# Optimization experiments

Measured on AMD Instinct MI355X. Metric: run time of the kernel, lower is better.

The kernel has to match this reference:

```python
import jax, jax.numpy as jnp
import numpy as np

N = 50000
E = 1600000
IN_DIM = 256
HID = 64
OUT = 16
NEG_SLOPE = 0.01


def setup_inputs() -> dict:
    key = jax.random.key(0)
    ks = jax.random.split(key, 6)
    local_features = jax.random.normal(ks[0], (N, IN_DIM), dtype=jnp.float32)
    edge_index = jax.random.randint(ks[1], (2, E), 0, N, dtype=jnp.int32)
    W0 = jax.random.normal(ks[2], (IN_DIM, HID), dtype=jnp.float32) * 0.05
    a0 = jax.random.normal(ks[3], (2 * HID, 1), dtype=jnp.float32) * 0.05
    W1 = jax.random.normal(ks[4], (HID, OUT), dtype=jnp.float32) * 0.05
    a1 = jax.random.normal(ks[5], (2 * OUT, 1), dtype=jnp.float32) * 0.05
    return {"local_features": local_features, "edge_index": edge_index,
            "W0": W0, "a0": a0, "W1": W1, "a1": a1}


def _segment_softmax(scores, seg, num_segments):
    # softmax over edges sharing the same row (destination) id
    smax = jax.ops.segment_max(scores, seg, num_segments=num_segments)
    ex = jnp.exp(scores - smax[seg])
    ssum = jax.ops.segment_sum(ex, seg, num_segments=num_segments)
    return ex / ssum[seg]


def _gat_layer(H, row, col, W, a, apply_elu):
    d = W.shape[1]
    Hw = H @ W                                   # [N, d]
    # score_e = leaky_relu([Hw[row] || Hw[col]] @ a) = leaky_relu(pr[row] + pc[col])
    pr = Hw @ a[:d, 0]                           # [N]
    pc = Hw @ a[d:, 0]                           # [N]
    s = pr[row] + pc[col]                        # [E]
    s = jnp.where(s >= 0, s, NEG_SLOPE * s)      # leaky_relu
    att = _segment_softmax(s, row, Hw.shape[0])  # per-row sparse softmax (dim=1)
    # out[row] = sum_e att_e * Hw[col_e]
    out = jax.ops.segment_sum(att[:, None] * Hw[col], row, num_segments=Hw.shape[0])
    if apply_elu:
        out = jnp.where(out > 0, out, jnp.expm1(out))  # elu
    return out


def reference(local_features, edge_index, W0, a0, W1, a1):
    row = edge_index[0]
    col = edge_index[1]
    H = _gat_layer(local_features, row, col, W0, a0, apply_elu=True)
    H = _gat_layer(H, row, col, W1, a1, apply_elu=False)
    return jax.nn.log_softmax(H, axis=1)
```

## Files before the change

### kernel.cpp

```cpp
#include <hip/hip_runtime.h>
#include <hip/hip_bf16.h>
#include <math.h>

#define NN 50000
#define NE 1600000
#define BSH 9
#define BCK 98
#define BCAP 20480

typedef __attribute__((ext_vector_type(8))) short bf16x8;
typedef __attribute__((ext_vector_type(4))) float f32x4;
typedef __attribute__((ext_vector_type(2))) float f32x2;

__device__ __forceinline__ short f2bf(float f) {
    return (short)((__float_as_uint(f) + 0x8000u) >> 16);
}
__device__ __forceinline__ float lo16(unsigned u) { return __uint_as_float(u << 16); }
__device__ __forceinline__ float hi16(unsigned u) { return __uint_as_float(u & 0xffff0000u); }
__device__ __forceinline__ unsigned enc_f(float f) {
    unsigned u = __float_as_uint(f);
    return (u & 0x80000000u) ? ~u : (u | 0x80000000u);
}
__device__ __forceinline__ float dec_f(unsigned e) {
    return (e & 0x80000000u) ? __uint_as_float(e & 0x7FFFFFFFu)
                             : __uint_as_float(~e);
}

__global__ void setup_kernel(int* __restrict__ gcursor, unsigned* __restrict__ maxes,
                             const float* __restrict__ W, ushort* __restrict__ WTg) {
    int b = blockIdx.x;
    int t = threadIdx.x;
    if (b == 0) {
        if (t < BCK) gcursor[t] = t * BCAP;
        if (t < 2) maxes[t] = 0u;
    } else {
        int i = (b - 1) * 256 + t;
        int n = i >> 8, k = i & 255;
        WTg[n * 264 + k] = (ushort)f2bf(W[k * 64 + n]);
    }
}

__global__ void __launch_bounds__(1024) binA_kernel(
        const int* __restrict__ row, const int* __restrict__ col,
        int* __restrict__ gcursor, unsigned* __restrict__ staging) {
    __shared__ unsigned lds_stage[8192];
    __shared__ unsigned lds_addr[8192];
    __shared__ int lds_cnt[128];
    __shared__ int lds_off[128];
    __shared__ int wg_goff[128];
    __shared__ int wtot[2];
    int t = threadIdx.x;
    int lane = t & 63;
    int w = t >> 6;

    for (int cb = blockIdx.x * 8192; cb < NE; cb += gridDim.x * 8192) {
        int cnt_edges = NE - cb; if (cnt_edges > 8192) cnt_edges = 8192;
        if (t < 128) lds_cnt[t] = 0;
        __syncthreads();
        int myb[8]; int mylo[8]; unsigned mypk[8];
        int e0 = cb + t * 8;
        if (t * 8 + 7 < cnt_edges) {
            int4 r0 = *(const int4*)(row + e0);
            int4 r1 = *(const int4*)(row + e0 + 4);
            int4 c0 = *(const int4*)(col + e0);
            int4 c1 = *(const int4*)(col + e0 + 4);
            int rr[8] = {r0.x, r0.y, r0.z, r0.w, r1.x, r1.y, r1.z, r1.w};
            int cc[8] = {c0.x, c0.y, c0.z, c0.w, c1.x, c1.y, c1.z, c1.w};
            #pragma unroll
            for (int i = 0; i < 8; ++i) {
                int b = rr[i] >> BSH;
                myb[i] = b;
                mypk[i] = ((unsigned)(rr[i] & 511) << 16) | (unsigned)cc[i];
                mylo[i] = atomicAdd(&lds_cnt[b], 1);
            }
        } else {
            #pragma unroll
            for (int i = 0; i < 8; ++i) {
                int idx = t * 8 + i;
                myb[i] = -1;
                if (idx < cnt_edges) {
                    int e = cb + idx;
                    int r = row[e], c = col[e];
                    myb[i] = r >> BSH;
                    mypk[i] = ((unsigned)(r & 511) << 16) | (unsigned)c;
                    mylo[i] = atomicAdd(&lds_cnt[myb[i]], 1);
                }
            }
        }
        __syncthreads();
        int v = (t < 128) ? lds_cnt[t] : 0;
        int x = v;
        #pragma unroll
        for (int off = 1; off < 64; off <<= 1) {
            int y = __shfl_up(x, off);
            if (lane >= off) x += y;
        }
        if (t < 128 && lane == 63) wtot[w] = x;
        __syncthreads();
        int add = (w == 1) ? wtot[0] : 0;
        if (t < 128) lds_off[t] = x - v + add;
        if (t < BCK) {
            int cc2 = lds_cnt[t];
            wg_goff[t] = cc2 ? atomicAdd(&gcursor[t], cc2) : 0;
        }
        __syncthreads();
        #pragma unroll
        for (int i = 0; i < 8; ++i) if (myb[i] >= 0) {
            int p = lds_off[myb[i]] + mylo[i];
            lds_stage[p] = mypk[i];
            lds_addr[p] = (unsigned)(wg_goff[myb[i]] + mylo[i]);
        }
        __syncthreads();
        for (int i = t; i < cnt_edges; i += 1024)
            staging[lds_addr[i]] = lds_stage[i];
        __syncthreads();
    }
}

__global__ void __launch_bounds__(1024) binB_kernel(
        const int* __restrict__ gcursor,
        const unsigned* __restrict__ staging,
        int* __restrict__ rowptr,
        ushort* __restrict__ colperm) {
    __shared__ int bsc[128];
    __shared__ int bw[2];
    __shared__ int cur[512];
    __shared__ int wls8[8];
    __shared__ ushort lds_col[BCAP];
    int b = blockIdx.x;
    int t = threadIdx.x;
    int lane = t & 63;
    int w = t >> 6;

    if (t < 128) {
        int v = 0;
        if (t < BCK) {
            v = gcursor[t] - t * BCAP;
            if (v > BCAP) v = BCAP;
        }
        int x = v;
        #pragma unroll
        for (int off = 1; off < 64; off <<= 1) {
            int y = __shfl_up(x, off);
            if (lane >= off) x += y;
        }
        if (lane == 63) bw[w] = x;
        bsc[t] = x - v;
    }
    __syncthreads();
    int gbase = bsc[b] + ((b >= 64) ? bw[0] : 0);
    int cnt = gcursor[b] - b * BCAP;
    if (cnt > BCAP) cnt = BCAP;
    if (b == 0 && t == 0) rowptr[NN] = bw[0] + bw[1];
    int rbase = b << BSH;
    int nrows = NN - rbase; if (nrows > 512) nrows = 512;
    const unsigned* sb = staging + (size_t)b * BCAP;

    unsigned ev[20];
    #pragma unroll
    for (int j = 0; j < 5; ++j) {
        int i0 = t * 4 + j * 4096;
        uint4 val = {0u, 0u, 0u, 0u};
        if (i0 + 3 < cnt) {
            val = *(const uint4*)(sb + i0);
        } else {
            if (i0 + 0 < cnt) val.x = sb[i0 + 0];
            if (i0 + 1 < cnt) val.y = sb[i0 + 1];
            if (i0 + 2 < cnt) val.z = sb[i0 + 2];
            if (i0 + 3 < cnt) val.w = sb[i0 + 3];
        }
        ev[j * 4 + 0] = val.x; ev[j * 4 + 1] = val.y;
        ev[j * 4 + 2] = val.z; ev[j * 4 + 3] = val.w;
    }

    if (t < 512) cur[t] = 0;
    __syncthreads();
    #pragma unroll
    for (int j = 0; j < 5; ++j) {
        #pragma unroll
        for (int l = 0; l < 4; ++l) {
            int idx = t * 4 + j * 4096 + l;
            if (idx < cnt) atomicAdd(&cur[ev[j * 4 + l] >> 16], 1);
        }
    }
    __syncthreads();
    int v = 0, x = 0;
    if (t < 512) {
        v = cur[t];
        x = v;
        #pragma unroll
        for (int off = 1; off < 64; off <<= 1) {
            int y = __shfl_up(x, off);
            if (lane >= off) x += y;
        }
        if (lane == 63) wls8[w] = x;
    }
    __syncthreads();
    if (t < 8) {
        int s = wls8[t];
        #pragma unroll
        for (int off = 1; off < 8; off <<= 1) {
            int y = __shfl_up(s, off, 8);
            if ((t & 7) >= off) s += y;
        }
        wls8[t] = s;
    }
    __syncthreads();
    int excl = 0;
    if (t < 512) {
        excl = x - v + ((w > 0) ? wls8[w - 1] : 0);
        if (t < nrows) rowptr[rbase + t] = gbase + excl;
    }
    __syncthreads();
    if (t < 512) cur[t] = excl;
    __syncthreads();
    #pragma unroll
    for (int j = 0; j < 5; ++j) {
        #pragma unroll
        for (int l = 0; l < 4; ++l) {
            int idx = t * 4 + j * 4096 + l;
            if (idx < cnt) {
                unsigned e = ev[j * 4 + l];
                int pos = atomicAdd(&cur[e >> 16], 1);
                lds_col[pos] = (ushort)(e & 0xFFFFu);
            }
        }
    }
    __syncthreads();
    for (int i = t; i < cnt; i += 1024)
        colperm[gbase + i] = lds_col[i];
}

__global__ void pcmax_kernel(const float* __restrict__ pc, unsigned* __restrict__ out) {
    int i = blockIdx.x * 256 + threadIdx.x;
    float v = (i < NN) ? pc[i] : -1e30f;
    #pragma unroll
    for (int off = 32; off; off >>= 1) v = fmaxf(v, __shfl_xor(v, off));
    if ((threadIdx.x & 63) == 0) atomicMax(out, enc_f(v));
}

__global__ void __launch_bounds__(256) gemm0_kernel(
        const float* __restrict__ X,
        const ushort* __restrict__ WTg,
        const float* __restrict__ a,
        __hip_bfloat16* __restrict__ Hwb,
        float* __restrict__ pr,
        float* __restrict__ pc,
        unsigned* __restrict__ max0) {
    __shared__ ushort Wt[64 * 264];
    __shared__ unsigned bmax;
    int tid = threadIdx.x;
    if (tid == 0) bmax = 0u;
    {
        const uint* src = (const uint*)WTg;
        uint* dst = (uint*)Wt;
        for (int i = tid; i < 64 * 132; i += 256) dst[i] = src[i];
    }
    __syncthreads();
    int lane = tid & 63, wid = tid >> 6;
    int c = lane & 15, quad = lane >> 4;
    const ushort* wtp[4];
#pragma unroll
    for (int g = 0; g < 4; ++g) wtp[g] = &Wt[(g * 16 + c) * 264 + quad * 8];
    float aA[4], aB[4];
#pragma unroll
    for (int g = 0; g < 4; ++g) { aA[g] = a[g * 16 + c]; aB[g] = a[64 + g * 16 + c]; }

    int row0 = blockIdx.x * 128 + wid * 16;
    float qmax = -1e30f;

#pragma unroll
    for (int tt = 0; tt < 2; ++tt) {
        int rt = row0 + tt * 64;
        int arow = rt + c; if (arow >= NN) arow = NN - 1;
        const float* xbase = X + (size_t)arow * 256 + quad * 8;
        f32x4 acc[4];
#pragma unroll
        for (int g = 0; g < 4; ++g) acc[g] = (f32x4){0.f, 0.f, 0.f, 0.f};

#pragma unroll
        for (int k0 = 0; k0 < 256; k0 += 32) {
            float4 xa = *(const float4*)(xbase + k0);
            float4 xb = *(const float4*)(xbase + k0 + 4);
            bf16x8 af;
            af[0] = f2bf(xa.x); af[1] = f2bf(xa.y); af[2] = f2bf(xa.z); af[3] = f2bf(xa.w);
            af[4] = f2bf(xb.x); af[5] = f2bf(xb.y); af[6] = f2bf(xb.z); af[7] = f2bf(xb.w);
#pragma unroll
            for (int g = 0; g < 4; ++g) {
                bf16x8 bg = *(const bf16x8*)(wtp[g] + k0);
                acc[g] = __builtin_amdgcn_mfma_f32_16x16x32_bf16(af, bg, acc[g], 0, 0, 0);
            }
        }

#pragma unroll
        for (int r = 0; r < 4; ++r) {
            int row = rt + quad * 4 + r;
            float v0 = acc[0][r], v1 = acc[1][r], v2 = acc[2][r], v3 = acc[3][r];
            if (row < NN) {
                __hip_bfloat16* hp = Hwb + (size_t)row * 64 + c;
                hp[0]  = __float2bfloat16(v0);
                hp[16] = __float2bfloat16(v1);
                hp[32] = __float2bfloat16(v2);
                hp[48] = __float2bfloat16(v3);
            }
            float pv = v0 * aA[0] + v1 * aA[1] + v2 * aA[2] + v3 * aA[3];
            float qv = v0 * aB[0] + v1 * aB[1] + v2 * aB[2] + v3 * aB[3];
#pragma unroll
            for (int off = 8; off; off >>= 1) {
                pv += __shfl_xor(pv, off);
                qv += __shfl_xor(qv, off);
            }
            if (c == 0 && row < NN) { pr[row] = pv; pc[row] = qv; }
            if (row < NN) qmax = fmaxf(qmax, qv);
        }
    }
    qmax = fmaxf(qmax, __shfl_xor(qmax, 16));
    qmax = fmaxf(qmax, __shfl_xor(qmax, 32));
    if (lane == 0) atomicMax(&bmax, enc_f(qmax));
    __syncthreads();
    if (tid == 0) atomicMax(max0, bmax);
}

__global__ void __launch_bounds__(256) node0_kernel(
        const int* __restrict__ rowptr,
        const ushort* __restrict__ colperm,
        const float* __restrict__ pr,
        const float* __restrict__ pc,
        const unsigned* __restrict__ pcmax,
        const ushort* __restrict__ Hwb,
        const float* __restrict__ W1,
        const float* __restrict__ a1,
        __hip_bfloat16* __restrict__ Hw1b,
        float* __restrict__ pr1,
        float* __restrict__ pc1) {
    __shared__ float W1s[64 * 17];
    __shared__ float a1s[32];
    __shared__ float hbuf[4][64];
    __shared__ unsigned long long wcbuf[4][64];
    int t = threadIdx.x;
    for (int i = t; i < 64 * 16; i += 256)
        W1s[(i >> 4) * 17 + (i & 15)] = W1[i];
    if (t < 32) a1s[t] = a1[t];
    __syncthreads();

    int lane = t & 63;
    int wid = t >> 6;
    int node = blockIdx.x * 4 + wid;
    int k = lane & 15, q = lane >> 4;
    int start = rowptr[node], end = rowptr[node + 1];
    float pri = pr[node];
    float m = pri + dec_f(*pcmax);
    m = (m >= 0.f) ? m : 0.01f * m;

    float wsum = 0.f;
    f32x2 accA = {0.f, 0.f}, accB = {0.f, 0.f};
    for (int base = start; base < end; base += 64) {
        int n = end - base; if (n > 64) n = 64;
        float wv = 0.f; unsigned cv = 0;
        if (lane < n) {
            cv = (unsigned)colperm[base + lane];
            float s = pri + pc[cv];
            s = (s >= 0.f) ? s : 0.01f * s;
            wv = __expf(s - m);
        }
        wsum += wv;
        wcbuf[wid][lane] = ((unsigned long long)cv << 32) |
                           (unsigned long long)__float_as_uint(wv);
        int iters = (n + 3) >> 2;
        #pragma unroll 4
        for (int jj = 0; jj < iters; ++jj) {
            unsigned long long wc = wcbuf[wid][jj * 4 + q];
            float wj = __uint_as_float((unsigned)wc);
            int cj = (int)(wc >> 32);
            uint2 hv = *(const uint2*)(Hwb + (size_t)cj * 64 + k * 4);
            f32x2 wj2 = {wj, wj};
            f32x2 h01 = {lo16(hv.x), hi16(hv.x)};
            f32x2 h23 = {lo16(hv.y), hi16(hv.y)};
            accA += wj2 * h01;
            accB += wj2 * h23;
        }
    }
#pragma unroll
    for (int off = 32; off; off >>= 1) wsum += __shfl_xor(wsum, off);
    float acc0 = accA.x, acc1 = accA.y, acc2 = accB.x, acc3 = accB.y;
    acc0 += __shfl_xor(acc0, 16); acc0 += __shfl_xor(acc0, 32);
    acc1 += __shfl_xor(acc1, 16); acc1 += __shfl_xor(acc1, 32);
    acc2 += __shfl_xor(acc2, 16); acc2 += __shfl_xor(acc2, 32);
    acc3 += __shfl_xor(acc3, 16); acc3 += __shfl_xor(acc3, 32);

    float inv = (wsum > 0.f) ? 1.f / wsum : 0.f;
    float h0 = acc0 * inv; h0 = (h0 > 0.f) ? h0 : (__expf(h0) - 1.f);
    float h1 = acc1 * inv; h1 = (h1 > 0.f) ? h1 : (__expf(h1) - 1.f);
    float h2 = acc2 * inv; h2 = (h2 > 0.f) ? h2 : (__expf(h2) - 1.f);
    float h3 = acc3 * inv; h3 = (h3 > 0.f) ? h3 : (__expf(h3) - 1.f);
    if (q == 0) {
        float4 hh = {h0, h1, h2, h3};
        *(float4*)&hbuf[wid][k * 4] = hh;
    }
    int j = lane & 15, p = lane >> 4;
    const float* hbp = hbuf[wid];
    float vj = 0.f;
#pragma unroll
    for (int i = 0; i < 16; ++i) {
        int kk = p * 16 + i;
        vj = fmaf(hbp[kk], W1s[kk * 17 + j], vj);
    }
    vj += __shfl_xor(vj, 16);
    vj += __shfl_xor(vj, 32);
    if (p == 0) Hw1b[(size_t)node * 16 + j] = __float2bfloat16(vj);
    float pv = vj * a1s[j];
    float qv = vj * a1s[16 + j];
#pragma unroll
    for (int off = 8; off; off >>= 1) {
        pv += __shfl_xor(pv, off);
        qv += __shfl_xor(qv, off);
    }
    if (lane == 0) { pr1[node] = pv; pc1[node] = qv; }
}

__global__ void __launch_bounds__(256) node1_kernel(
        const int* __restrict__ rowptr,
        const ushort* __restrict__ colperm,
        const float* __restrict__ pr,
        const float* __restrict__ pc,
        const unsigned* __restrict__ pcmax,
        const ushort* __restrict__ Hwb,
        float* __restrict__ out) {
    __shared__ unsigned long long wcbuf[4][64];
    int lane = threadIdx.x & 63;
    int wid = threadIdx.x >> 6;
    int node = blockIdx.x * 4 + wid;
    int k = lane & 7, q = lane >> 3;
    int start = rowptr[node], end = rowptr[node + 1];
    float pri = pr[node];
    float m = pri + dec_f(*pcmax);
    m = (m >= 0.f) ? m : 0.01f * m;

    float wsum = 0.f;
    f32x2 acc = {0.f, 0.f};
    for (int base = start; base < end; base += 64) {
        int n = end - base; if (n > 64) n = 64;
        float wv = 0.f; unsigned cv = 0;
        if (lane < n) {
            cv = (unsigned)colperm[base + lane];
            float s = pri + pc[cv];
            s = (s >= 0.f) ? s : 0.01f * s;
            wv = __expf(s - m);
        }
        wsum += wv;
        wcbuf[wid][lane] = ((unsigned long long)cv << 32) |
                           (unsigned long long)__float_as_uint(wv);
        int iters = (n + 7) >> 3;
        #pragma unroll 8
        for (int jj = 0; jj < iters; ++jj) {
            unsigned long long wc = wcbuf[wid][jj * 8 + q];
            float wj = __uint_as_float((unsigned)wc);
            int cj = (int)(wc >> 32);
            unsigned hv = *(const unsigned*)(Hwb + (size_t)cj * 16 + k * 2);
            f32x2 wj2 = {wj, wj};
            f32x2 h = {lo16(hv), hi16(hv)};
            acc += wj2 * h;
        }
    }
#pragma unroll
    for (int off = 32; off; off >>= 1) wsum += __shfl_xor(wsum, off);
    float a0 = acc.x, a1 = acc.y;
    a0 += __shfl_xor(a0, 8); a0 += __shfl_xor(a0, 16); a0 += __shfl_xor(a0, 32);
    a1 += __shfl_xor(a1, 8); a1 += __shfl_xor(a1, 16); a1 += __shfl_xor(a1, 32);
    float inv = (wsum > 0.f) ? 1.f / wsum : 0.f;
    float v0 = a0 * inv, v1 = a1 * inv;
    float mm = fmaxf(v0, v1);
#pragma unroll
    for (int off = 1; off < 8; off <<= 1) mm = fmaxf(mm, __shfl_xor(mm, off, 8));
    float ssx = __expf(v0 - mm) + __expf(v1 - mm);
#pragma unroll
    for (int off = 1; off < 8; off <<= 1) ssx += __shfl_xor(ssx, off, 8);
    float lse = mm + __logf(ssx);
    if (q == 0) {
        float2 o = {v0 - lse, v1 - lse};
        *(float2*)(out + (size_t)node * 16 + k * 2) = o;
    }
}

extern "C" void kernel_launch(void* const* d_in, const int* in_sizes, int n_in,
                              void* d_out, int out_size, void* d_ws, size_t ws_size,
                              hipStream_t stream) {
    const float* X  = (const float*)d_in[0];
    const int*   ei = (const int*)d_in[1];
    const float* W0 = (const float*)d_in[2];
    const float* a0 = (const float*)d_in[3];
    const float* W1 = (const float*)d_in[4];
    const float* a1 = (const float*)d_in[5];
    float* out = (float*)d_out;

    const int* row = ei;
    const int* col = ei + NE;

    char* wsb = (char*)d_ws;
    size_t off = 0;
    auto alloc = [&](size_t bytes) {
        void* p = wsb + off;
        off += (bytes + 15) & ~(size_t)15;
        return p;
    };
    unsigned* maxes = (unsigned*)alloc(16);
    int* rowptr     = (int*)alloc((NN + 2) * 4);
    int* gcursor    = (int*)alloc(128 * 4);
    unsigned* staging = (unsigned*)alloc((size_t)BCK * BCAP * 4);
    ushort* colperm = (ushort*)alloc((size_t)NE * 2);
    ushort* WTg     = (ushort*)alloc((size_t)64 * 264 * 2);
    __hip_bfloat16* Hw0b = (__hip_bfloat16*)alloc((size_t)NN * 64 * 2);
    float* pr0      = (float*)alloc(NN * 4);
    float* pc0      = (float*)alloc(NN * 4);
    __hip_bfloat16* Hw1b = (__hip_bfloat16*)alloc((size_t)NN * 16 * 2);
    float* pr1      = (float*)alloc(NN * 4);
    float* pc1      = (float*)alloc(NN * 4);

    setup_kernel<<<65, 256, 0, stream>>>(gcursor, maxes, W0, WTg);
    binA_kernel<<<196, 1024, 0, stream>>>(row, col, gcursor, staging);
    binB_kernel<<<BCK, 1024, 0, stream>>>(gcursor, staging, rowptr, colperm);

    gemm0_kernel<<<(NN + 127) / 128, 256, 0, stream>>>(X, WTg, a0, Hw0b, pr0, pc0,
                                                       &maxes[0]);
    node0_kernel<<<NN / 4, 256, 0, stream>>>(rowptr, colperm, pr0, pc0,
                                             &maxes[0], (const ushort*)Hw0b,
                                             W1, a1, Hw1b, pr1, pc1);

    pcmax_kernel<<<(NN + 255) / 256, 256, 0, stream>>>(pc1, &maxes[1]);
    node1_kernel<<<NN / 4, 256, 0, stream>>>(rowptr, colperm, pr1, pc1,
                                             &maxes[1], (const ushort*)Hw1b, out);
}
```

Baseline: 213.8 us.

## Batch neighbor gathers for memory-level parallelism and fuse pc1 max into node0

The gather loops in both aggregation kernels now issue eight independent row loads per batch before doing any FMAs. Column indices and weights are staged in separate LDS arrays, and out-of-range slots are clamped and given zero weight. This is meant to hide gather latency by keeping more loads in flight. The separate pcmax kernel is removed and its max reduction is folded into node0 through a block-level LDS atomic and one global atomic per block, which saves a launch and a pass over pc1 at the cost of extra registers and redundant loads on the padding slots.

```diff
diff --git a/kernel.cpp b/kernel.cpp
--- a/kernel.cpp
+++ b/kernel.cpp
@@ -231,14 +231,6 @@
         colperm[gbase + i] = lds_col[i];
 }
 
-__global__ void pcmax_kernel(const float* __restrict__ pc, unsigned* __restrict__ out) {
-    int i = blockIdx.x * 256 + threadIdx.x;
-    float v = (i < NN) ? pc[i] : -1e30f;
-    #pragma unroll
-    for (int off = 32; off; off >>= 1) v = fmaxf(v, __shfl_xor(v, off));
-    if ((threadIdx.x & 63) == 0) atomicMax(out, enc_f(v));
-}
-
 __global__ void __launch_bounds__(256) gemm0_kernel(
         const float* __restrict__ X,
         const ushort* __restrict__ WTg,
@@ -332,12 +324,16 @@
         const float* __restrict__ a1,
         __hip_bfloat16* __restrict__ Hw1b,
         float* __restrict__ pr1,
-        float* __restrict__ pc1) {
+        float* __restrict__ pc1,
+        unsigned* __restrict__ max1) {
     __shared__ float W1s[64 * 17];
     __shared__ float a1s[32];
     __shared__ float hbuf[4][64];
-    __shared__ unsigned long long wcbuf[4][64];
+    __shared__ float wbuf[4][64];
+    __shared__ int   cbuf[4][64];
+    __shared__ unsigned bmax1;
     int t = threadIdx.x;
+    if (t == 0) bmax1 = 0u;
     for (int i = t; i < 64 * 16; i += 256)
         W1s[(i >> 4) * 17 + (i & 15)] = W1[i];
     if (t < 32) a1s[t] = a1[t];
@@ -356,28 +352,38 @@
     f32x2 accA = {0.f, 0.f}, accB = {0.f, 0.f};
     for (int base = start; base < end; base += 64) {
         int n = end - base; if (n > 64) n = 64;
-        float wv = 0.f; unsigned cv = 0;
+        float wv = 0.f; int cv = 0;
         if (lane < n) {
-            cv = (unsigned)colperm[base + lane];
+            cv = (int)colperm[base + lane];
             float s = pri + pc[cv];
             s = (s >= 0.f) ? s : 0.01f * s;
             wv = __expf(s - m);
         }
         wsum += wv;
-        wcbuf[wid][lane] = ((unsigned long long)cv << 32) |
-                           (unsigned long long)__float_as_uint(wv);
+        wbuf[wid][lane] = wv;
+        cbuf[wid][lane] = cv;
         int iters = (n + 3) >> 2;
-        #pragma unroll 4
-        for (int jj = 0; jj < iters; ++jj) {
-            unsigned long long wc = wcbuf[wid][jj * 4 + q];
-            float wj = __uint_as_float((unsigned)wc);
-            int cj = (int)(wc >> 32);
-            uint2 hv = *(const uint2*)(Hwb + (size_t)cj * 64 + k * 4);
-            f32x2 wj2 = {wj, wj};
-            f32x2 h01 = {lo16(hv.x), hi16(hv.x)};
-            f32x2 h23 = {lo16(hv.y), hi16(hv.y)};
-            accA += wj2 * h01;
-            accB += wj2 * h23;
+        for (int jj = 0; jj < iters; jj += 8) {
+            int cjr[8]; uint2 hv[8];
+            #pragma unroll
+            for (int u = 0; u < 8; ++u) {
+                int idx = jj + u; if (idx >= iters) idx = iters - 1;
+                cjr[u] = cbuf[wid][idx * 4 + q];
+            }
+            #pragma unroll
+            for (int u = 0; u < 8; ++u)
+                hv[u] = *(const uint2*)(Hwb + (size_t)cjr[u] * 64 + k * 4);
+            #pragma unroll
+            for (int u = 0; u < 8; ++u) {
+                int idx = jj + u; if (idx >= iters) idx = iters - 1;
+                float wj = wbuf[wid][idx * 4 + q];
+                wj = (jj + u < iters) ? wj : 0.f;
+                f32x2 wj2 = {wj, wj};
+                f32x2 h01 = {lo16(hv[u].x), hi16(hv[u].x)};
+                f32x2 h23 = {lo16(hv[u].y), hi16(hv[u].y)};
+                accA += wj2 * h01;
+                accB += wj2 * h23;
+            }
         }
     }
 #pragma unroll
@@ -415,7 +421,12 @@
         pv += __shfl_xor(pv, off);
         qv += __shfl_xor(qv, off);
     }
-    if (lane == 0) { pr1[node] = pv; pc1[node] = qv; }
+    if (lane == 0) {
+        pr1[node] = pv; pc1[node] = qv;
+        atomicMax(&bmax1, enc_f(qv));
+    }
+    __syncthreads();
+    if (t == 0) atomicMax(max1, bmax1);
 }
 
 __global__ void __launch_bounds__(256) node1_kernel(
@@ -426,7 +437,8 @@
         const unsigned* __restrict__ pcmax,
         const ushort* __restrict__ Hwb,
         float* __restrict__ out) {
-    __shared__ unsigned long long wcbuf[4][64];
+    __shared__ float wbuf[4][64];
+    __shared__ int   cbuf[4][64];
     int lane = threadIdx.x & 63;
     int wid = threadIdx.x >> 6;
     int node = blockIdx.x * 4 + wid;
@@ -440,25 +452,33 @@
     f32x2 acc = {0.f, 0.f};
     for (int base = start; base < end; base += 64) {
         int n = end - base; if (n > 64) n = 64;
-        float wv = 0.f; unsigned cv = 0;
+        float wv = 0.f; int cv = 0;
         if (lane < n) {
-            cv = (unsigned)colperm[base + lane];
+            cv = (int)colperm[base + lane];
             float s = pri + pc[cv];
             s = (s >= 0.f) ? s : 0.01f * s;
             wv = __expf(s - m);
         }
         wsum += wv;
-        wcbuf[wid][lane] = ((unsigned long long)cv << 32) |
-                           (unsigned long long)__float_as_uint(wv);
+        wbuf[wid][lane] = wv;
+        cbuf[wid][lane] = cv;
         int iters = (n + 7) >> 3;
-        #pragma unroll 8
-        for (int jj = 0; jj < iters; ++jj) {
-            unsigned long long wc = wcbuf[wid][jj * 8 + q];
-            float wj = __uint_as_float((unsigned)wc);
-            int cj = (int)(wc >> 32);
-            unsigned hv = *(const unsigned*)(Hwb + (size_t)cj * 16 + k * 2);
+        int cjr[8]; unsigned hv[8];
+        #pragma unroll
+        for (int u = 0; u < 8; ++u) {
+            int idx = u; if (idx >= iters) idx = iters - 1;
+            cjr[u] = cbuf[wid][idx * 8 + q];
+        }
+        #pragma unroll
+        for (int u = 0; u < 8; ++u)
+            hv[u] = *(const unsigned*)(Hwb + (size_t)cjr[u] * 16 + k * 2);
+        #pragma unroll
+        for (int u = 0; u < 8; ++u) {
+            int idx = u; if (idx >= iters) idx = iters - 1;
+            float wj = wbuf[wid][idx * 8 + q];
+            wj = (u < iters) ? wj : 0.f;
             f32x2 wj2 = {wj, wj};
-            f32x2 h = {lo16(hv), hi16(hv)};
+            f32x2 h = {lo16(hv[u]), hi16(hv[u])};
             acc += wj2 * h;
         }
     }
@@ -524,9 +544,8 @@
                                                        &maxes[0]);
     node0_kernel<<<NN / 4, 256, 0, stream>>>(rowptr, colperm, pr0, pc0,
                                              &maxes[0], (const ushort*)Hw0b,
-                                             W1, a1, Hw1b, pr1, pc1);
-
-    pcmax_kernel<<<(NN + 255) / 256, 256, 0, stream>>>(pc1, &maxes[1]);
+                                             W1, a1, Hw1b, pr1, pc1, &maxes[1]);
+
     node1_kernel<<<NN / 4, 256, 0, stream>>>(rowptr, colperm, pr1, pc1,
                                              &maxes[1], (const ushort*)Hw1b, out);
 }
```

Result: slower. 305.6 us (+42.9%).
